# Kernel tuning notes

Measured on AMD Instinct MI355X. Metric: run time of the kernel, lower is better.

Reference implementation:

```python
import jax, jax.numpy as jnp
import numpy as np

B, T, H, DEPTH = 16, 2048, 256, 3

def setup_inputs() -> dict:
    key = jax.random.key(0)
    ks = jax.random.split(key, 5)
    x = jax.random.normal(ks[0], (B, T, H), dtype=jnp.float32)
    seq_lens = jax.random.randint(ks[1], (B,), 1, T + 1, dtype=jnp.int32)
    s = 1.0 / np.sqrt(H)
    W_ih = jax.random.uniform(ks[2], (DEPTH, H, H), jnp.float32, -s, s)
    W_hh = jax.random.uniform(ks[3], (DEPTH, H, H), jnp.float32, -s, s)
    b = jax.random.uniform(ks[4], (DEPTH, H), jnp.float32, -s, s)
    return {"x": x, "seq_lens": seq_lens, "W_ih": W_ih, "W_hh": W_hh, "b": b}

def reference(x, seq_lens, W_ih, W_hh, b):
    # x: [B, T, D], stacked depth-3 single-state recurrent cells:
    #   h[t,k] = tanh(inp @ W_ih[k]^T + h[t-1,k] @ W_hh[k]^T + b[k])
    # where inp = x[t] for k==0 else h[t,k-1]; h[-1,k] = 0 (init_state).
    Bx, Tx, D = x.shape
    depth = W_ih.shape[0]
    h0 = jnp.zeros((depth, Bx, D), dtype=x.dtype)

    def step(h_prev, x_t):  # h_prev: [depth, B, H], x_t: [B, D]
        inp = x_t
        hs = []
        for k in range(depth):
            hk = jnp.tanh(inp @ W_ih[k].T + h_prev[k] @ W_hh[k].T + b[k])
            hs.append(hk)
            inp = hk
        h_new = jnp.stack(hs)  # [depth, B, H]
        return h_new, h_new

    _, ys = jax.lax.scan(step, h0, jnp.swapaxes(x, 0, 1))  # ys: [T, depth, B, H]
    out = jnp.transpose(ys, (2, 0, 1, 3))  # [B, T, depth, H]
    # positions past each sequence's length are never written (stay zero)
    mask = (jnp.arange(Tx)[None, :] < seq_lens[:, None])[:, :, None, None]
    return out * mask.astype(out.dtype)
```

## Files before the change

kernel.cpp:

```cpp
#include <hip/hip_runtime.h>
#include <stdint.h>


#define TT 2048
#define HH 256

typedef _Float16 h16x8 __attribute__((ext_vector_type(8)));
typedef float f32x4 __attribute__((ext_vector_type(4)));

__device__ __forceinline__ unsigned pkrtz(float a, float b) {
  return __builtin_bit_cast(unsigned, __builtin_amdgcn_cvt_pkrtz(a, b));
}

__device__ __forceinline__ float tanh_fast(float x) {
  float xm = fmaxf(x, -15.0f);
  float e = __builtin_amdgcn_exp2f(xm * -2.88539008177793f);
  float r = __builtin_amdgcn_rcpf(1.0f + e);
  return __builtin_fmaf(-2.0f * e, r, 1.0f);
}

__device__ __forceinline__ void spin_ge(int* p, int need) {
  while (__hip_atomic_load(p, __ATOMIC_ACQUIRE, __HIP_MEMORY_SCOPE_AGENT) < need)
    __builtin_amdgcn_s_sleep(2);
}

__global__ __launch_bounds__(512, 2)
void stacked_rnn(const float* __restrict__ x,
                 const int* __restrict__ seq_lens,
                 const float* __restrict__ Wih,
                 const float* __restrict__ Whh,
                 const float* __restrict__ bias,
                 float* __restrict__ out,
                 int* flags) {
  const int ks = blockIdx.x;
  const int tid = (int)threadIdx.x;
  const int w = tid >> 6;
  const int lane = tid & 63;
  const int q = lane >> 4;
  const int n = lane & 15;

  __shared__ unsigned short Bsm[2][8192];

  int* flag_up = flags + (ks - 1) * 64;
  int* flag_me = flags + ks * 64;

  h16x8 wf[2][16];
  {
    const float* wih_s = Wih + ks * (HH * HH);
    const float* whh_s = Whh + ks * (HH * HH);
#pragma unroll
    for (int mti = 0; mti < 2; ++mti) {
      const int fA = w * 32 + mti * 16 + n;
#pragma unroll
      for (int kt = 0; kt < 16; ++kt) {
        const int col = (kt & 7) * 32 + q * 8;
        const float* src = (kt < 8) ? (wih_s + fA * HH + col)
                                    : (whh_s + fA * HH + col);
        float4 a0 = ((const float4*)src)[0];
        float4 a1 = ((const float4*)src)[1];
        h16x8 f;
        f[0] = (_Float16)a0.x; f[1] = (_Float16)a0.y;
        f[2] = (_Float16)a0.z; f[3] = (_Float16)a0.w;
        f[4] = (_Float16)a1.x; f[5] = (_Float16)a1.y;
        f[6] = (_Float16)a1.z; f[7] = (_Float16)a1.w;
        wf[mti][kt] = f;
      }
    }
  }

  f32x4 biasv[2];
#pragma unroll
  for (int mti = 0; mti < 2; ++mti)
#pragma unroll
    for (int r = 0; r < 4; ++r)
      biasv[mti][r] = bias[ks * HH + w * 32 + mti * 16 + q * 4 + r];

  const int sl = seq_lens[n];

  const int rdE = (q * 16 + (n ^ q)) * 8;
  const int rdO = (q * 16 + (n ^ q ^ 4)) * 8;

  int hofs[2];
#pragma unroll
  for (int mti = 0; mti < 2; ++mti) {
    const int u = (8 + w) * 4 + mti * 2 + (q >> 1);
    hofs[mti] = (u * 16 + (n ^ (u & 7))) * 8 + (q & 1) * 4;
  }

  const int n_l = tid >> 5;
  const int k8  = tid & 31;
  const int u_l = (k8 >> 2) * 4 + (k8 & 3);
  const int ldst = (u_l * 16 + (n_l ^ (u_l & 7))) * 8;

  const float* src_base;
  int src_stride;
  if (ks == 0) {
    src_base = x + ((n_l * TT) << 8) + (k8 << 3);
    src_stride = HH;
  } else {
    src_base = out + (((n_l * TT) * 3 + (ks - 1)) << 8) + (k8 << 3);
    src_stride = 3 * HH;
  }

  for (int i = tid; i < 4096; i += 512) Bsm[0][4096 + i] = 0;
  if (ks > 0 && tid == 0) spin_ge(flag_up, 18);
  __syncthreads();

  {
    float4 c0 = ((const float4*)src_base)[0];
    float4 c1 = ((const float4*)src_base)[1];
    *(uint4*)&Bsm[0][ldst] = make_uint4(pkrtz(c0.x, c0.y), pkrtz(c0.z, c0.w),
                                        pkrtz(c1.x, c1.y), pkrtz(c1.z, c1.w));
  }
  float4 pfB0 = ((const float4*)(src_base + src_stride))[0];
  float4 pfB1 = ((const float4*)(src_base + src_stride))[1];
  const float* src_pf = src_base + 2 * src_stride;
  __syncthreads();

  float* outp = out + ((n * TT) * 3 + ks) * HH + w * 32 + q * 4;

  for (int t = 0; t < TT; ++t) {
    unsigned short* Bp = Bsm[t & 1];
    unsigned short* Bq = Bsm[(t & 1) ^ 1];

    if ((t & 7) == 0 && t > 0 && ks < 2 && tid == 0)
      __hip_atomic_store(flag_me, t, __ATOMIC_RELEASE,
                         __HIP_MEMORY_SCOPE_AGENT);
    if ((t & 15) == 0 && t > 0 && ks > 0) {
      if (tid == 0) {
        int need = t + 18;
        if (need > TT) need = TT;
        spin_ge(flag_up, need);
      }
      __syncthreads();
    }

    float4 pfA0, pfA1;
    const bool more2 = (t + 2 < TT);
    if (more2) {
      pfA0 = ((const float4*)src_pf)[0];
      pfA1 = ((const float4*)src_pf)[1];
    }
    src_pf += src_stride;

    f32x4 acc[2] = {biasv[0], biasv[1]};
#pragma unroll
    for (int kt = 0; kt < 16; ++kt) {
      const int ofs = ((kt & 1) ? rdO : rdE) + kt * 512;
      h16x8 bf = *(const h16x8*)&Bp[ofs];
      acc[0] = __builtin_amdgcn_mfma_f32_16x16x32_f16(wf[0][kt], bf, acc[0], 0, 0, 0);
      acc[1] = __builtin_amdgcn_mfma_f32_16x16x32_f16(wf[1][kt], bf, acc[1], 0, 0, 0);
    }

    const bool live = (t < sl);
    uint2 hpk[2];
#pragma unroll
    for (int mti = 0; mti < 2; ++mti) {
      float h0 = tanh_fast(acc[mti][0]);
      float h1 = tanh_fast(acc[mti][1]);
      float h2 = tanh_fast(acc[mti][2]);
      float h3 = tanh_fast(acc[mti][3]);
      hpk[mti].x = pkrtz(h0, h1);
      hpk[mti].y = pkrtz(h2, h3);
      float4 od;
      od.x = live ? h0 : 0.0f;
      od.y = live ? h1 : 0.0f;
      od.z = live ? h2 : 0.0f;
      od.w = live ? h3 : 0.0f;
      *(float4*)(outp + mti * 16) = od;
    }
    outp += 3 * HH;

    if (t + 1 < TT) {
      *(uint4*)&Bq[ldst] = make_uint4(pkrtz(pfB0.x, pfB0.y), pkrtz(pfB0.z, pfB0.w),
                                      pkrtz(pfB1.x, pfB1.y), pkrtz(pfB1.z, pfB1.w));
      *(uint2*)&Bq[hofs[0]] = hpk[0];
      *(uint2*)&Bq[hofs[1]] = hpk[1];
      if (more2) { pfB0 = pfA0; pfB1 = pfA1; }
    }

    __syncthreads();
  }

  if (ks < 2 && tid == 0)
    __hip_atomic_store(flag_me, TT, __ATOMIC_RELEASE, __HIP_MEMORY_SCOPE_AGENT);
}

extern "C" void kernel_launch(void* const* d_in, const int* in_sizes, int n_in,
                              void* d_out, int out_size, void* d_ws, size_t ws_size,
                              hipStream_t stream) {
  (void)in_sizes; (void)n_in; (void)out_size; (void)ws_size;
  const float* x   = (const float*)d_in[0];
  const int*   sl  = (const int*)d_in[1];
  const float* wih = (const float*)d_in[2];
  const float* whh = (const float*)d_in[3];
  const float* b   = (const float*)d_in[4];

  (void)hipMemsetAsync(d_ws, 0, 1024, stream);
  hipLaunchKernelGGL(stacked_rnn, dim3(3), dim3(512), 0, stream,
                     x, sl, wih, whh, b, (float*)d_out, (int*)d_ws);
}
```

Measured before the change: 2.305 ms.

## Halve block to 4 waves with 4 M-tiles each and overlap tanh with MFMAs

Each block now runs 256 threads, with every wave holding four 16-row weight tiles in registers instead of two. The tanh of the first two tiles is interleaved with the MFMAs of the last two, and the output store is deferred by one step so it sits off the critical path. Input prefetch is issued inside the MMA loop and packed early. The aim is to shorten the per-timestep latency of the serial recurrence through fewer waves per barrier and better overlap. The cost is much higher register pressure (64 h16x8 weight fragments plus the B fragments), and the flag protocol is adjusted to publish t-1 to match the delayed stores.

After: 3.230 ms. +40.1%, slower.

```diff
diff --git a/kernel.cpp b/kernel.cpp
--- a/kernel.cpp
+++ b/kernel.cpp
@@ -24,7 +24,7 @@
     __builtin_amdgcn_s_sleep(2);
 }
 
-__global__ __launch_bounds__(512, 2)
+__global__ __launch_bounds__(256, 1)
 void stacked_rnn(const float* __restrict__ x,
                  const int* __restrict__ seq_lens,
                  const float* __restrict__ Wih,
@@ -39,18 +39,18 @@
   const int q = lane >> 4;
   const int n = lane & 15;
 
-  __shared__ unsigned short Bsm[2][8192];
+  __shared__ __align__(16) unsigned short Bsm[2][8192];
 
   int* flag_up = flags + (ks - 1) * 64;
   int* flag_me = flags + ks * 64;
 
-  h16x8 wf[2][16];
+  h16x8 wf[4][16];
   {
     const float* wih_s = Wih + ks * (HH * HH);
     const float* whh_s = Whh + ks * (HH * HH);
 #pragma unroll
-    for (int mti = 0; mti < 2; ++mti) {
-      const int fA = w * 32 + mti * 16 + n;
+    for (int mti = 0; mti < 4; ++mti) {
+      const int fA = w * 64 + mti * 16 + n;
 #pragma unroll
       for (int kt = 0; kt < 16; ++kt) {
         const int col = (kt & 7) * 32 + q * 8;
@@ -68,63 +68,83 @@
     }
   }
 
-  f32x4 biasv[2];
-#pragma unroll
-  for (int mti = 0; mti < 2; ++mti)
+  f32x4 biasv[4];
+#pragma unroll
+  for (int mti = 0; mti < 4; ++mti)
 #pragma unroll
     for (int r = 0; r < 4; ++r)
-      biasv[mti][r] = bias[ks * HH + w * 32 + mti * 16 + q * 4 + r];
+      biasv[mti][r] = bias[ks * HH + w * 64 + mti * 16 + q * 4 + r];
 
   const int sl = seq_lens[n];
 
   const int rdE = (q * 16 + (n ^ q)) * 8;
   const int rdO = (q * 16 + (n ^ q ^ 4)) * 8;
 
-  int hofs[2];
-#pragma unroll
-  for (int mti = 0; mti < 2; ++mti) {
-    const int u = (8 + w) * 4 + mti * 2 + (q >> 1);
+  int hofs[4];
+#pragma unroll
+  for (int mti = 0; mti < 4; ++mti) {
+    const int u = (8 + 2 * w + (mti >> 1)) * 4 + 2 * (mti & 1) + (q >> 1);
     hofs[mti] = (u * 16 + (n ^ (u & 7))) * 8 + (q & 1) * 4;
   }
 
-  const int n_l = tid >> 5;
-  const int k8  = tid & 31;
-  const int u_l = (k8 >> 2) * 4 + (k8 & 3);
-  const int ldst = (u_l * 16 + (n_l ^ (u_l & 7))) * 8;
-
-  const float* src_base;
+  const int n0 = tid >> 5;
+  const int k8 = tid & 31;
+  const int uL = (k8 >> 2) * 4 + (k8 & 3);
+  const int ldstA = (uL * 16 + (n0 ^ (uL & 7))) * 8;
+  const int ldstB = (uL * 16 + ((n0 + 8) ^ (uL & 7))) * 8;
+
+  const float* srcA;
+  const float* srcB;
   int src_stride;
   if (ks == 0) {
-    src_base = x + ((n_l * TT) << 8) + (k8 << 3);
+    srcA = x + ((n0 * TT) << 8) + (k8 << 3);
+    srcB = x + (((n0 + 8) * TT) << 8) + (k8 << 3);
     src_stride = HH;
   } else {
-    src_base = out + (((n_l * TT) * 3 + (ks - 1)) << 8) + (k8 << 3);
+    srcA = out + (((n0 * TT) * 3 + (ks - 1)) << 8) + (k8 << 3);
+    srcB = out + ((((n0 + 8) * TT) * 3 + (ks - 1)) << 8) + (k8 << 3);
     src_stride = 3 * HH;
   }
 
-  for (int i = tid; i < 4096; i += 512) Bsm[0][4096 + i] = 0;
+#pragma unroll
+  for (int i = 0; i < 2; ++i)
+    ((uint4*)&Bsm[0][4096])[tid + 256 * i] = make_uint4(0, 0, 0, 0);
   if (ks > 0 && tid == 0) spin_ge(flag_up, 18);
   __syncthreads();
 
+  uint4 ipkA, ipkB;
   {
-    float4 c0 = ((const float4*)src_base)[0];
-    float4 c1 = ((const float4*)src_base)[1];
-    *(uint4*)&Bsm[0][ldst] = make_uint4(pkrtz(c0.x, c0.y), pkrtz(c0.z, c0.w),
-                                        pkrtz(c1.x, c1.y), pkrtz(c1.z, c1.w));
-  }
-  float4 pfB0 = ((const float4*)(src_base + src_stride))[0];
-  float4 pfB1 = ((const float4*)(src_base + src_stride))[1];
-  const float* src_pf = src_base + 2 * src_stride;
+    float4 a0 = ((const float4*)srcA)[0];
+    float4 a1 = ((const float4*)srcA)[1];
+    *(uint4*)&Bsm[0][ldstA] = make_uint4(pkrtz(a0.x, a0.y), pkrtz(a0.z, a0.w),
+                                         pkrtz(a1.x, a1.y), pkrtz(a1.z, a1.w));
+    float4 b0 = ((const float4*)srcB)[0];
+    float4 b1 = ((const float4*)srcB)[1];
+    *(uint4*)&Bsm[0][ldstB] = make_uint4(pkrtz(b0.x, b0.y), pkrtz(b0.z, b0.w),
+                                         pkrtz(b1.x, b1.y), pkrtz(b1.z, b1.w));
+    float4 c0 = ((const float4*)(srcA + src_stride))[0];
+    float4 c1 = ((const float4*)(srcA + src_stride))[1];
+    ipkA = make_uint4(pkrtz(c0.x, c0.y), pkrtz(c0.z, c0.w),
+                      pkrtz(c1.x, c1.y), pkrtz(c1.z, c1.w));
+    float4 d0 = ((const float4*)(srcB + src_stride))[0];
+    float4 d1 = ((const float4*)(srcB + src_stride))[1];
+    ipkB = make_uint4(pkrtz(d0.x, d0.y), pkrtz(d0.z, d0.w),
+                      pkrtz(d1.x, d1.y), pkrtz(d1.z, d1.w));
+  }
+  const float* pfsA = srcA + 2 * src_stride;
+  const float* pfsB = srcB + 2 * src_stride;
   __syncthreads();
 
-  float* outp = out + ((n * TT) * 3 + ks) * HH + w * 32 + q * 4;
+  float* outp_st = out + ((n * TT) * 3 + ks) * HH + w * 64 + q * 4;
+  float hv[16];
+  bool lp = true;
 
   for (int t = 0; t < TT; ++t) {
     unsigned short* Bp = Bsm[t & 1];
     unsigned short* Bq = Bsm[(t & 1) ^ 1];
 
     if ((t & 7) == 0 && t > 0 && ks < 2 && tid == 0)
-      __hip_atomic_store(flag_me, t, __ATOMIC_RELEASE,
+      __hip_atomic_store(flag_me, t - 1, __ATOMIC_RELEASE,
                          __HIP_MEMORY_SCOPE_AGENT);
     if ((t & 15) == 0 && t > 0 && ks > 0) {
       if (tid == 0) {
@@ -135,53 +155,86 @@
       __syncthreads();
     }
 
-    float4 pfA0, pfA1;
     const bool more2 = (t + 2 < TT);
-    if (more2) {
-      pfA0 = ((const float4*)src_pf)[0];
-      pfA1 = ((const float4*)src_pf)[1];
-    }
-    src_pf += src_stride;
-
-    f32x4 acc[2] = {biasv[0], biasv[1]};
+    float4 pfA0, pfA1, pfA2, pfA3;
+
+    h16x8 bfr[16];
+    f32x4 acc[4] = {biasv[0], biasv[1], biasv[2], biasv[3]};
+
 #pragma unroll
     for (int kt = 0; kt < 16; ++kt) {
       const int ofs = ((kt & 1) ? rdO : rdE) + kt * 512;
-      h16x8 bf = *(const h16x8*)&Bp[ofs];
-      acc[0] = __builtin_amdgcn_mfma_f32_16x16x32_f16(wf[0][kt], bf, acc[0], 0, 0, 0);
-      acc[1] = __builtin_amdgcn_mfma_f32_16x16x32_f16(wf[1][kt], bf, acc[1], 0, 0, 0);
-    }
-
-    const bool live = (t < sl);
-    uint2 hpk[2];
-#pragma unroll
-    for (int mti = 0; mti < 2; ++mti) {
-      float h0 = tanh_fast(acc[mti][0]);
-      float h1 = tanh_fast(acc[mti][1]);
-      float h2 = tanh_fast(acc[mti][2]);
-      float h3 = tanh_fast(acc[mti][3]);
-      hpk[mti].x = pkrtz(h0, h1);
-      hpk[mti].y = pkrtz(h2, h3);
-      float4 od;
-      od.x = live ? h0 : 0.0f;
-      od.y = live ? h1 : 0.0f;
-      od.z = live ? h2 : 0.0f;
-      od.w = live ? h3 : 0.0f;
-      *(float4*)(outp + mti * 16) = od;
-    }
-    outp += 3 * HH;
+      bfr[kt] = *(const h16x8*)&Bp[ofs];
+      acc[0] = __builtin_amdgcn_mfma_f32_16x16x32_f16(wf[0][kt], bfr[kt], acc[0], 0, 0, 0);
+      acc[1] = __builtin_amdgcn_mfma_f32_16x16x32_f16(wf[1][kt], bfr[kt], acc[1], 0, 0, 0);
+      if (kt == 0 && more2) {
+        pfA0 = ((const float4*)pfsA)[0];
+        pfA1 = ((const float4*)pfsA)[1];
+        pfA2 = ((const float4*)pfsB)[0];
+        pfA3 = ((const float4*)pfsB)[1];
+      }
+    }
+    pfsA += src_stride;
+    pfsB += src_stride;
+
+    if (t) {
+#pragma unroll
+      for (int mti = 0; mti < 4; ++mti) {
+        float4 od;
+        od.x = lp ? hv[mti * 4 + 0] : 0.0f;
+        od.y = lp ? hv[mti * 4 + 1] : 0.0f;
+        od.z = lp ? hv[mti * 4 + 2] : 0.0f;
+        od.w = lp ? hv[mti * 4 + 3] : 0.0f;
+        *(float4*)(outp_st + mti * 16) = od;
+      }
+      outp_st += 3 * HH;
+    }
+
+    uint2 hpk[4];
+#pragma unroll
+    for (int kt = 0; kt < 16; ++kt) {
+      acc[2] = __builtin_amdgcn_mfma_f32_16x16x32_f16(wf[2][kt], bfr[kt], acc[2], 0, 0, 0);
+      acc[3] = __builtin_amdgcn_mfma_f32_16x16x32_f16(wf[3][kt], bfr[kt], acc[3], 0, 0, 0);
+      if (kt < 8) hv[kt] = tanh_fast(acc[kt >> 2][kt & 3]);
+      if (kt == 8)  { hpk[0].x = pkrtz(hv[0], hv[1]); hpk[0].y = pkrtz(hv[2], hv[3]); }
+      if (kt == 9)  { hpk[1].x = pkrtz(hv[4], hv[5]); hpk[1].y = pkrtz(hv[6], hv[7]); }
+    }
+
+#pragma unroll
+    for (int j = 0; j < 8; ++j) hv[8 + j] = tanh_fast(acc[2 + (j >> 2)][j & 3]);
+    hpk[2].x = pkrtz(hv[8], hv[9]);
+    hpk[2].y = pkrtz(hv[10], hv[11]);
+    hpk[3].x = pkrtz(hv[12], hv[13]);
+    hpk[3].y = pkrtz(hv[14], hv[15]);
 
     if (t + 1 < TT) {
-      *(uint4*)&Bq[ldst] = make_uint4(pkrtz(pfB0.x, pfB0.y), pkrtz(pfB0.z, pfB0.w),
-                                      pkrtz(pfB1.x, pfB1.y), pkrtz(pfB1.z, pfB1.w));
+      *(uint4*)&Bq[ldstA] = ipkA;
+      *(uint4*)&Bq[ldstB] = ipkB;
       *(uint2*)&Bq[hofs[0]] = hpk[0];
       *(uint2*)&Bq[hofs[1]] = hpk[1];
-      if (more2) { pfB0 = pfA0; pfB1 = pfA1; }
-    }
-
+      *(uint2*)&Bq[hofs[2]] = hpk[2];
+      *(uint2*)&Bq[hofs[3]] = hpk[3];
+    }
+    if (more2) {
+      ipkA = make_uint4(pkrtz(pfA0.x, pfA0.y), pkrtz(pfA0.z, pfA0.w),
+                        pkrtz(pfA1.x, pfA1.y), pkrtz(pfA1.z, pfA1.w));
+      ipkB = make_uint4(pkrtz(pfA2.x, pfA2.y), pkrtz(pfA2.z, pfA2.w),
+                        pkrtz(pfA3.x, pfA3.y), pkrtz(pfA3.z, pfA3.w));
+    }
+    lp = (t < sl);
     __syncthreads();
   }
 
+#pragma unroll
+  for (int mti = 0; mti < 4; ++mti) {
+    float4 od;
+    od.x = lp ? hv[mti * 4 + 0] : 0.0f;
+    od.y = lp ? hv[mti * 4 + 1] : 0.0f;
+    od.z = lp ? hv[mti * 4 + 2] : 0.0f;
+    od.w = lp ? hv[mti * 4 + 3] : 0.0f;
+    *(float4*)(outp_st + mti * 16) = od;
+  }
+  __syncthreads();
   if (ks < 2 && tid == 0)
     __hip_atomic_store(flag_me, TT, __ATOMIC_RELEASE, __HIP_MEMORY_SCOPE_AGENT);
 }
@@ -197,6 +250,6 @@
   const float* b   = (const float*)d_in[4];
 
   (void)hipMemsetAsync(d_ws, 0, 1024, stream);
-  hipLaunchKernelGGL(stacked_rnn, dim3(3), dim3(512), 0, stream,
+  hipLaunchKernelGGL(stacked_rnn, dim3(3), dim3(256), 0, stream,
                      x, sl, wih, whh, b, (float*)d_out, (int*)d_ws);
 }
```
